# Kernel tuning notes

Measured on AMD Instinct MI355X. Metric: run time of the kernel, lower is better.

The kernel has to match this reference:

```python
import jax, jax.numpy as jnp
import numpy as np

H = 640          # hidden_size
E = 5            # num_experts
R = 8            # rank
K = 2            # top_k
ROUTER_HID = 256
SCALING = 16.0 / R  # alpha / rank


def setup_inputs() -> dict:
    key = jax.random.key(0)
    ks = jax.random.split(key, 8)
    B, S = 8, 4096
    x = jax.random.normal(ks[0], (B, S, H), dtype=jnp.float32)
    base_output = jax.random.normal(ks[1], (B, S, H), dtype=jnp.float32)
    # router params
    W1 = jax.random.normal(ks[2], (H, ROUTER_HID), dtype=jnp.float32) * (1.0 / np.sqrt(H))
    b1 = jnp.zeros((ROUTER_HID,), dtype=jnp.float32)
    W2 = jax.random.normal(ks[3], (ROUTER_HID, E), dtype=jnp.float32) * (1.0 / np.sqrt(ROUTER_HID))
    b2 = jnp.zeros((E,), dtype=jnp.float32)
    # LoRA expert params (A ~ randn/rank as in torch init; B randn so output is nonzero for testing)
    A = jax.random.normal(ks[4], (E, H, R), dtype=jnp.float32) * (1.0 / R)
    Bm = jax.random.normal(ks[5], (E, R, H), dtype=jnp.float32) * 0.02
    return {"x": x, "base_output": base_output, "W1": W1, "b1": b1,
            "W2": W2, "b2": b2, "A": A, "Bm": Bm}


def reference(x, base_output, W1, b1, W2, b2, A, Bm):
    # Router: Linear -> SiLU -> Linear -> softmax
    h = jax.nn.silu(x @ W1 + b1)                       # [B,S,256]
    routing_weights = jax.nn.softmax(h @ W2 + b2, axis=-1)  # [B,S,E]
    top_w, top_idx = jax.lax.top_k(routing_weights, K)      # [B,S,K]
    top_w = top_w / jnp.sum(top_w, axis=-1, keepdims=True)
    # Dense all-expert LoRA outputs (faithful to torch.stack over experts)
    low = jnp.einsum('bsh,ehr->bser', x, A)            # [B,S,E,R]
    expert_outputs = jnp.einsum('bser,erh->bseh', low, Bm) * SCALING  # [B,S,E,H]
    # Gather top-k experts and combine
    gathered = jnp.take_along_axis(expert_outputs, top_idx[..., None], axis=2)  # [B,S,K,H]
    combined = jnp.sum(gathered * top_w[..., None], axis=2)  # [B,S,H]
    return base_output + combined
```

## Files before the change

### kernel.cpp

```cpp
#include <hip/hip_runtime.h>
#include <cstdint>
#include <cstddef>

#define H      640
#define RH     256
#define NE     5
#define NA     40
#define NTOK   32768
#define SCAL   2.0f
#define BK     16
#define BM     32

__device__ __forceinline__ float4 ld4(const float* p) {
    return *reinterpret_cast<const float4*>(p);
}

__global__ __launch_bounds__(256, 4)
void k_router(const float* __restrict__ x, const float* __restrict__ W1,
              const float* __restrict__ b1v, const float* __restrict__ W2,
              const float* __restrict__ b2v, const float* __restrict__ A,
              float* __restrict__ route_c, int* __restrict__ route_idx)
{
    __shared__ float xs[BM][20];
    __shared__ float ws[BK][RH];
    __shared__ float as_[BK][64];
    __shared__ float w2s[RH * NE];
    __shared__ float b1s[RH];
    __shared__ float low_lds[BM][NA];
    __shared__ float logit_lds[BM][8];

    const int tid  = threadIdx.x;
    const int row0 = blockIdx.x * BM;
    const int tm   = tid >> 4;
    const int tn   = tid & 15;

    for (int i = tid; i < RH * NE; i += 256) w2s[i] = W2[i];
    if (tid < RH) b1s[tid] = b1v[tid];

    float acc[2][16];
    #pragma unroll
    for (int j = 0; j < 2; j++)
        #pragma unroll
        for (int c = 0; c < 16; c++) acc[j][c] = 0.f;
    float accl[2][4];
    #pragma unroll
    for (int j = 0; j < 2; j++)
        #pragma unroll
        for (int c = 0; c < 4; c++) accl[j][c] = 0.f;

    for (int k0 = 0; k0 < H; k0 += BK) {
        __syncthreads();
        if (tid < 128) {
            int m = tid >> 2, c = tid & 3;
            *reinterpret_cast<float4*>(&xs[m][c * 4]) =
                ld4(x + (size_t)(row0 + m) * H + k0 + c * 4);
        }
        #pragma unroll
        for (int i = 0; i < 4; i++) {
            int idx4 = tid + i * 256;
            int row = idx4 >> 6, c4 = idx4 & 63;
            *reinterpret_cast<float4*>(&ws[row][c4 * 4]) =
                ld4(W1 + (size_t)(k0 + row) * RH + c4 * 4);
        }
        if (tid < 160) {
            int row = tid / 10, c4 = tid % 10;
            int e = c4 >> 1, r0 = (c4 & 1) * 4;
            *reinterpret_cast<float4*>(&as_[row][c4 * 4]) =
                ld4(A + ((size_t)e * H + k0 + row) * 8 + r0);
        }
        __syncthreads();

        #pragma unroll
        for (int kk4 = 0; kk4 < BK; kk4 += 4) {
            float4 xa0 = *reinterpret_cast<const float4*>(&xs[2 * tm + 0][kk4]);
            float4 xa1 = *reinterpret_cast<const float4*>(&xs[2 * tm + 1][kk4]);
            #pragma unroll
            for (int u = 0; u < 4; u++) {
                float bb[16];
                #pragma unroll
                for (int q = 0; q < 4; q++)
                    *reinterpret_cast<float4*>(&bb[q * 4]) =
                        *reinterpret_cast<const float4*>(&ws[kk4 + u][(tn + 16 * q) * 4]);
                float lb[4];
                *reinterpret_cast<float4*>(lb) =
                    *reinterpret_cast<const float4*>(&as_[kk4 + u][tn * 4]);
                float av0 = (u == 0) ? xa0.x : (u == 1) ? xa0.y : (u == 2) ? xa0.z : xa0.w;
                float av1 = (u == 0) ? xa1.x : (u == 1) ? xa1.y : (u == 2) ? xa1.z : xa1.w;
                #pragma unroll
                for (int c = 0; c < 16; c++) {
                    acc[0][c] = fmaf(av0, bb[c], acc[0][c]);
                    acc[1][c] = fmaf(av1, bb[c], acc[1][c]);
                }
                #pragma unroll
                for (int c = 0; c < 4; c++) {
                    accl[0][c] = fmaf(av0, lb[c], accl[0][c]);
                    accl[1][c] = fmaf(av1, lb[c], accl[1][c]);
                }
            }
        }
    }

    if (tn < 10) {
        #pragma unroll
        for (int j = 0; j < 2; j++)
            *reinterpret_cast<float4*>(&low_lds[2 * tm + j][tn * 4]) =
                *reinterpret_cast<float4*>(&accl[j][0]);
    }

    float part[2][5];
    #pragma unroll
    for (int j = 0; j < 2; j++)
        #pragma unroll
        for (int e = 0; e < 5; e++) part[j][e] = 0.f;

    #pragma unroll
    for (int q = 0; q < 4; q++)
        #pragma unroll
        for (int i4 = 0; i4 < 4; i4++) {
            int col = (tn + 16 * q) * 4 + i4;
            float bbias = b1s[col];
            float w2r[5];
            #pragma unroll
            for (int e = 0; e < 5; e++) w2r[e] = w2s[col * 5 + e];
            #pragma unroll
            for (int j = 0; j < 2; j++) {
                float v = acc[j][q * 4 + i4] + bbias;
                float s = __fdividef(v, 1.f + __expf(-v));
                #pragma unroll
                for (int e = 0; e < 5; e++) part[j][e] = fmaf(s, w2r[e], part[j][e]);
            }
        }

    #pragma unroll
    for (int j = 0; j < 2; j++)
        #pragma unroll
        for (int e = 0; e < 5; e++) {
            float v = part[j][e];
            v += __shfl_xor(v, 1);
            v += __shfl_xor(v, 2);
            v += __shfl_xor(v, 4);
            v += __shfl_xor(v, 8);
            part[j][e] = v;
        }

    if (tn == 0) {
        #pragma unroll
        for (int j = 0; j < 2; j++)
            #pragma unroll
            for (int e = 0; e < 5; e++) logit_lds[2 * tm + j][e] = part[j][e];
    }
    __syncthreads();

    if (tid < BM) {
        const int t = tid;
        float l0 = logit_lds[t][0] + b2v[0];
        float l1 = logit_lds[t][1] + b2v[1];
        float l2 = logit_lds[t][2] + b2v[2];
        float l3 = logit_lds[t][3] + b2v[3];
        float l4 = logit_lds[t][4] + b2v[4];
        int   i0 = 0;  float m0 = l0;
        int   i1 = -1; float m1 = -3.4e38f;
        if (l1 > m0) { m1 = m0; i1 = i0; m0 = l1; i0 = 1; } else if (l1 > m1) { m1 = l1; i1 = 1; }
        if (l2 > m0) { m1 = m0; i1 = i0; m0 = l2; i0 = 2; } else if (l2 > m1) { m1 = l2; i1 = 2; }
        if (l3 > m0) { m1 = m0; i1 = i0; m0 = l3; i0 = 3; } else if (l3 > m1) { m1 = l3; i1 = 3; }
        if (l4 > m0) { m1 = m0; i1 = i0; m0 = l4; i0 = 4; } else if (l4 > m1) { m1 = l4; i1 = 4; }
        float w1r = __expf(m1 - m0);
        float inv = __fdividef(1.f, 1.f + w1r);
        float c0 = inv * SCAL;
        float c1 = w1r * inv * SCAL;
        int gt = row0 + t;
        #pragma unroll
        for (int r4 = 0; r4 < 2; r4++) {
            float4 v0 = ld4(&low_lds[t][i0 * 8 + r4 * 4]);
            v0.x *= c0; v0.y *= c0; v0.z *= c0; v0.w *= c0;
            *reinterpret_cast<float4*>(&route_c[(size_t)gt * 16 + r4 * 4]) = v0;
            float4 v1 = ld4(&low_lds[t][i1 * 8 + r4 * 4]);
            v1.x *= c1; v1.y *= c1; v1.z *= c1; v1.w *= c1;
            *reinterpret_cast<float4*>(&route_c[(size_t)gt * 16 + 8 + r4 * 4]) = v1;
        }
        route_idx[gt * 2 + 0] = i0;
        route_idx[gt * 2 + 1] = i1;
    }
}

__global__ __launch_bounds__(512)
void k_combine(const float* __restrict__ base, const float* __restrict__ Bm,
               const float* __restrict__ route_c, const int* __restrict__ route_idx,
               float* __restrict__ out)
{
    __shared__ float bs[NA][H];
    const int tid = threadIdx.x;
    for (int i4 = tid; i4 < NA * H / 4; i4 += 512)
        reinterpret_cast<float4*>(&bs[0][0])[i4] = reinterpret_cast<const float4*>(Bm)[i4];
    __syncthreads();

    const int w    = tid >> 6;
    const int lane = tid & 63;

    for (int it = 0; it < 16; it++) {
        int t = blockIdx.x * 128 + w * 16 + it;
        t = __builtin_amdgcn_readfirstlane(t);
        const int e0 = route_idx[t * 2 + 0];
        const int e1 = route_idx[t * 2 + 1];
        float cc[16];
        #pragma unroll
        for (int q = 0; q < 4; q++)
            *reinterpret_cast<float4*>(&cc[q * 4]) = ld4(route_c + (size_t)t * 16 + q * 4);

        const float* brow0 = &bs[e0 * 8][0];
        const float* brow1 = &bs[e1 * 8][0];
        const float* bp = base + (size_t)t * H;
        float*       op = out  + (size_t)t * H;

        #pragma unroll
        for (int i = 0; i < 2; i++) {
            int h = i * 256 + lane * 4;
            float4 a = ld4(bp + h);
            #pragma unroll
            for (int j = 0; j < 8; j++) {
                float4 bv = *reinterpret_cast<const float4*>(brow0 + j * H + h);
                a.x = fmaf(cc[j], bv.x, a.x); a.y = fmaf(cc[j], bv.y, a.y);
                a.z = fmaf(cc[j], bv.z, a.z); a.w = fmaf(cc[j], bv.w, a.w);
            }
            #pragma unroll
            for (int j = 0; j < 8; j++) {
                float4 bv = *reinterpret_cast<const float4*>(brow1 + j * H + h);
                a.x = fmaf(cc[8 + j], bv.x, a.x); a.y = fmaf(cc[8 + j], bv.y, a.y);
                a.z = fmaf(cc[8 + j], bv.z, a.z); a.w = fmaf(cc[8 + j], bv.w, a.w);
            }
            *reinterpret_cast<float4*>(op + h) = a;
        }
        {
            int h = 512 + lane * 2;
            float2 a = *reinterpret_cast<const float2*>(bp + h);
            #pragma unroll
            for (int j = 0; j < 8; j++) {
                float2 bv = *reinterpret_cast<const float2*>(brow0 + j * H + h);
                a.x = fmaf(cc[j], bv.x, a.x); a.y = fmaf(cc[j], bv.y, a.y);
            }
            #pragma unroll
            for (int j = 0; j < 8; j++) {
                float2 bv = *reinterpret_cast<const float2*>(brow1 + j * H + h);
                a.x = fmaf(cc[8 + j], bv.x, a.x); a.y = fmaf(cc[8 + j], bv.y, a.y);
            }
            *reinterpret_cast<float2*>(op + h) = a;
        }
    }
}

extern "C" void kernel_launch(void* const* d_in, const int* in_sizes, int n_in,
                              void* d_out, int out_size, void* d_ws, size_t ws_size,
                              hipStream_t stream)
{
    const float* x  = (const float*)d_in[0];
    const float* bo = (const float*)d_in[1];
    const float* W1 = (const float*)d_in[2];
    const float* b1 = (const float*)d_in[3];
    const float* W2 = (const float*)d_in[4];
    const float* b2 = (const float*)d_in[5];
    const float* A  = (const float*)d_in[6];
    const float* Bm = (const float*)d_in[7];
    float* out = (float*)d_out;

    float* route_c   = (float*)d_ws;
    int*   route_idx = (int*)((char*)d_ws + (size_t)NTOK * 16 * 4);

    k_router<<<dim3(NTOK / BM), dim3(256), 0, stream>>>(
        x, W1, b1, W2, b2, A, route_c, route_idx);
    k_combine<<<dim3(256), dim3(512), 0, stream>>>(
        bo, Bm, route_c, route_idx, out);
}
```

Measured before the change: 236.6 us.

## Prefetch router tiles into registers and load W1 directly to LDS

Restructures the router GEMM loop so the next K-tile of x and A is loaded into registers while the current tile is computed, then written to LDS after a barrier. The W1 tile is fetched with global_load_lds, which writes straight to LDS without passing through VGPRs. Shared buffers are aliased into one pool to cut LDS use, and the occupancy hint in launch_bounds is dropped. The aim is to hide global load latency behind the FMA loop, at the cost of extra registers and no double-buffering of the W1 LDS tile.

```diff
diff --git a/kernel.cpp b/kernel.cpp
--- a/kernel.cpp
+++ b/kernel.cpp
@@ -10,33 +10,62 @@
 #define SCAL   2.0f
 #define BK     16
 #define BM     32
+#define NT     (H / BK)
 
 __device__ __forceinline__ float4 ld4(const float* p) {
     return *reinterpret_cast<const float4*>(p);
 }
 
-__global__ __launch_bounds__(256, 4)
+__device__ __forceinline__ void gload16(const float* g, float* lds_base) {
+    __builtin_amdgcn_global_load_lds(
+        (const __attribute__((address_space(1))) void*)g,
+        (__attribute__((address_space(3))) void*)lds_base, 16, 0, 0);
+}
+
+__global__ __launch_bounds__(256)
 void k_router(const float* __restrict__ x, const float* __restrict__ W1,
               const float* __restrict__ b1v, const float* __restrict__ W2,
               const float* __restrict__ b2v, const float* __restrict__ A,
               float* __restrict__ route_c, int* __restrict__ route_idx)
 {
-    __shared__ float xs[BM][20];
     __shared__ float ws[BK][RH];
-    __shared__ float as_[BK][64];
     __shared__ float w2s[RH * NE];
     __shared__ float b1s[RH];
-    __shared__ float low_lds[BM][NA];
-    __shared__ float logit_lds[BM][8];
+    __shared__ __align__(16) char pool[6400];
+    float (*xs)[20]       = reinterpret_cast<float (*)[20]>(pool);
+    float (*as_)[NA]      = reinterpret_cast<float (*)[NA]>(pool + 2560);
+    float (*low_lds)[NA]  = reinterpret_cast<float (*)[NA]>(pool);
+    float (*logit_lds)[8] = reinterpret_cast<float (*)[8]>(pool + 5120);
 
     const int tid  = threadIdx.x;
     const int row0 = blockIdx.x * BM;
     const int tm   = tid >> 4;
     const int tn   = tid & 15;
+    const int lane = tid & 63;
+    const int wv   = tid >> 6;
+
+    const int xrow = tid >> 2, xc = tid & 3;
+    const int arow = tid / 10, ac4 = tid % 10;
+    const int ae = ac4 >> 1, ar0 = (ac4 & 1) * 4;
+    const float* xsrc = x + (size_t)(row0 + xrow) * H + xc * 4;
+    const float* asrc = A + ((size_t)ae * H + arow) * 8 + ar0;
 
     for (int i = tid; i < RH * NE; i += 256) w2s[i] = W2[i];
     if (tid < RH) b1s[tid] = b1v[tid];
 
+    #pragma unroll
+    for (int i = 0; i < 4; i++)
+        gload16(W1 + (size_t)(wv * 4 + i) * RH + lane * 4, &ws[wv * 4 + i][0]);
+    if (tid < 128) {
+        float4 xr = ld4(xsrc);
+        *reinterpret_cast<float4*>(&xs[xrow][xc * 4]) = xr;
+    }
+    if (tid < 160) {
+        float4 ar = ld4(asrc);
+        *reinterpret_cast<float4*>(&as_[arow][ac4 * 4]) = ar;
+    }
+    __syncthreads();
+
     float acc[2][16];
     #pragma unroll
     for (int j = 0; j < 2; j++)
@@ -48,27 +77,14 @@
         #pragma unroll
         for (int c = 0; c < 4; c++) accl[j][c] = 0.f;
 
-    for (int k0 = 0; k0 < H; k0 += BK) {
-        __syncthreads();
-        if (tid < 128) {
-            int m = tid >> 2, c = tid & 3;
-            *reinterpret_cast<float4*>(&xs[m][c * 4]) =
-                ld4(x + (size_t)(row0 + m) * H + k0 + c * 4);
-        }
-        #pragma unroll
-        for (int i = 0; i < 4; i++) {
-            int idx4 = tid + i * 256;
-            int row = idx4 >> 6, c4 = idx4 & 63;
-            *reinterpret_cast<float4*>(&ws[row][c4 * 4]) =
-                ld4(W1 + (size_t)(k0 + row) * RH + c4 * 4);
-        }
-        if (tid < 160) {
-            int row = tid / 10, c4 = tid % 10;
-            int e = c4 >> 1, r0 = (c4 & 1) * 4;
-            *reinterpret_cast<float4*>(&as_[row][c4 * 4]) =
-                ld4(A + ((size_t)e * H + k0 + row) * 8 + r0);
-        }
-        __syncthreads();
+    for (int t = 0; t < NT; ++t) {
+        const bool more = (t + 1 < NT);
+        const int k0n = (t + 1) * BK;
+        float4 xr, ar;
+        if (more) {
+            if (tid < 128) xr = ld4(xsrc + k0n);
+            if (tid < 160) ar = ld4(asrc + (size_t)k0n * 8);
+        }
 
         #pragma unroll
         for (int kk4 = 0; kk4 < BK; kk4 += 4) {
@@ -98,6 +114,19 @@
                 }
             }
         }
+
+        __syncthreads();
+        if (more) {
+            #pragma unroll
+            for (int i = 0; i < 4; i++)
+                gload16(W1 + ((size_t)k0n + wv * 4 + i) * RH + lane * 4,
+                        &ws[wv * 4 + i][0]);
+            if (tid < 128)
+                *reinterpret_cast<float4*>(&xs[xrow][xc * 4]) = xr;
+            if (tid < 160)
+                *reinterpret_cast<float4*>(&as_[arow][ac4 * 4]) = ar;
+        }
+        __syncthreads();
     }
 
     if (tn < 10) {
@@ -152,12 +181,12 @@
     __syncthreads();
 
     if (tid < BM) {
-        const int t = tid;
-        float l0 = logit_lds[t][0] + b2v[0];
-        float l1 = logit_lds[t][1] + b2v[1];
-        float l2 = logit_lds[t][2] + b2v[2];
-        float l3 = logit_lds[t][3] + b2v[3];
-        float l4 = logit_lds[t][4] + b2v[4];
+        const int tk = tid;
+        float l0 = logit_lds[tk][0] + b2v[0];
+        float l1 = logit_lds[tk][1] + b2v[1];
+        float l2 = logit_lds[tk][2] + b2v[2];
+        float l3 = logit_lds[tk][3] + b2v[3];
+        float l4 = logit_lds[tk][4] + b2v[4];
         int   i0 = 0;  float m0 = l0;
         int   i1 = -1; float m1 = -3.4e38f;
         if (l1 > m0) { m1 = m0; i1 = i0; m0 = l1; i0 = 1; } else if (l1 > m1) { m1 = l1; i1 = 1; }
@@ -168,13 +197,13 @@
         float inv = __fdividef(1.f, 1.f + w1r);
         float c0 = inv * SCAL;
         float c1 = w1r * inv * SCAL;
-        int gt = row0 + t;
+        int gt = row0 + tk;
         #pragma unroll
         for (int r4 = 0; r4 < 2; r4++) {
-            float4 v0 = ld4(&low_lds[t][i0 * 8 + r4 * 4]);
+            float4 v0 = ld4(&low_lds[tk][i0 * 8 + r4 * 4]);
             v0.x *= c0; v0.y *= c0; v0.z *= c0; v0.w *= c0;
             *reinterpret_cast<float4*>(&route_c[(size_t)gt * 16 + r4 * 4]) = v0;
-            float4 v1 = ld4(&low_lds[t][i1 * 8 + r4 * 4]);
+            float4 v1 = ld4(&low_lds[tk][i1 * 8 + r4 * 4]);
             v1.x *= c1; v1.y *= c1; v1.z *= c1; v1.w *= c1;
             *reinterpret_cast<float4*>(&route_c[(size_t)gt * 16 + 8 + r4 * 4]) = v1;
         }
```

New measurement: 396.7 us. +67.7%, slower.
